# Kernel optimization log

Measured on AMD Instinct MI355X. Metric: run time of the kernel, lower is better.

Reference implementation:

```python
import jax, jax.numpy as jnp
import numpy as np

B = 512      # batch = envs * nagents
M = 32       # nmodels
NAG = 8      # nagents
H = 256      # hidsz
NACT = 16    # nactions


def _lm(x, W, b, ids):
    # LinearMulti: per-example weight selected by model id.
    # x: [B, I], W: [M, I, O], b: [M, O], ids: [B] -> [B, O]
    return jnp.einsum('bi,bio->bo', x, W[ids]) + b[ids]


def setup_inputs() -> dict:
    key = jax.random.key(0)
    ks = jax.random.split(key, 16)
    s = 0.02
    return {
        'comm_in': jax.random.normal(ks[0], (B, NAG, H), jnp.float32),
        'inp': jnp.zeros((B, 1), jnp.int32),  # Embedding table has 1 row -> only index 0 valid
        'prev_hid': jax.random.normal(ks[1], (B, H), jnp.float32),
        'prev_cell': jnp.zeros((B, H), jnp.float32),  # unused in rnn branch, kept for signature fidelity
        'model_ids': jax.random.randint(ks[2], (B,), 0, M),
        # comm2hid LinearMulti (comm_encoder): hidsz -> hidsz
        'Wc': jax.random.normal(ks[3], (M, H, H), jnp.float32) * s,
        'bc': jax.random.normal(ks[4], (M, H), jnp.float32) * s,
        # rnn LinearMulti: hidsz -> hidsz
        'Wr': jax.random.normal(ks[5], (M, H, H), jnp.float32) * s,
        'br': jax.random.normal(ks[6], (M, H), jnp.float32) * s,
        # action LinearMulti: hidsz -> nactions
        'Wa': jax.random.normal(ks[7], (M, H, NACT), jnp.float32) * s,
        'ba': jax.random.normal(ks[8], (M, NACT), jnp.float32) * s,
        # baseline LinearMulti: hidsz -> 1
        'Wb': jax.random.normal(ks[9], (M, H, 1), jnp.float32) * s,
        'bb': jax.random.normal(ks[10], (M, 1), jnp.float32) * s,
        # comm_out LinearMulti (fully_connected): hidsz -> hidsz * nagents
        'Wo': jax.random.normal(ks[11], (M, H, H * NAG), jnp.float32) * s,
        'bo': jax.random.normal(ks[12], (M, H * NAG), jnp.float32) * s,
        # Encoder: Embedding(1, hidsz) + bias
        'lut': jax.random.normal(ks[13], (1, H), jnp.float32) * s,
        'enc_bias': jax.random.normal(ks[14], (H,), jnp.float32) * s,
    }


def reference(comm_in, inp, prev_hid, prev_cell, model_ids,
              Wc, bc, Wr, br, Wa, ba, Wb, bb, Wo, bo, lut, enc_bias):
    # __comm2hid: sum agent messages, then model-id-routed linear
    comm2hid = _lm(jnp.sum(comm_in, axis=1), Wc, bc, model_ids)  # [B, H]
    # Encoder: embedding lookup, sum over token dim, add bias
    enc = jnp.sum(lut[inp], axis=1) + enc_bias                   # [B, H]
    # _rnn: sum of encoder, routed recurrent linear, and comm; tanh gate
    hidstate = jnp.tanh(enc + _lm(prev_hid, Wr, br, model_ids) + comm2hid)
    # __action
    action_prob = jax.nn.softmax(_lm(hidstate, Wa, ba, model_ids), axis=-1)  # [B, NACT]
    baseline = _lm(hidstate, Wb, bb, model_ids)                              # [B, 1]
    # __comm_out (fully_connected): routed linear then divide by nagents-1
    comm_out = _lm(hidstate, Wo, bo, model_ids) / (NAG - 1)                  # [B, H*NAG]
    return (action_prob, baseline, hidstate, comm_out)
```

## Files before the change

kernel.cpp:

```cpp
#include <hip/hip_runtime.h>


constexpr int Bn = 512, Mn = 32, NAGn = 8, Hn = 256, NACTn = 16;
constexpr int On = Hn * NAGn;
constexpr int En = 32;
constexpr int EW = 8;

__device__ __forceinline__ void gl_lds16(const float* g, float* l) {
  __builtin_amdgcn_global_load_lds(
      (const __attribute__((address_space(1))) void*)g,
      (__attribute__((address_space(3))) void*)l, 16, 0, 0);
}


__global__ __launch_bounds__(512) void k_group(const int* __restrict__ ids,
                                               int* __restrict__ list32) {
  __shared__ int scnt[Mn];
  int t = threadIdx.x;
  if (t < Mn) scnt[t] = 0;
  list32[t] = -1;
  list32[t + 512] = -1;
  __syncthreads();
  int m = ids[t];
  int pos = atomicAdd(&scnt[m], 1);
  if (pos < En) list32[m * En + pos] = t;
}

__global__ __launch_bounds__(256) void k_pack(
    const float* __restrict__ comm_in, const float* __restrict__ prev_hid,
    const int* __restrict__ list32, float* __restrict__ xcat) {
  int m = blockIdx.x, half = blockIdx.y;
  int tid = threadIdx.x;
  __shared__ float buf[En][Hn + 1];
  __shared__ int lst[En];
  if (tid < En) lst[tid] = list32[m * En + tid];
  __syncthreads();
  if (half == 0) {
    for (int j = 0; j < En; j++) {
      int e = lst[j];
      float s = 0.f;
      if (e >= 0) {
        const float* cp = comm_in + (size_t)e * NAGn * Hn + tid;
#pragma unroll
        for (int a = 0; a < NAGn; a++) s += cp[a * Hn];
      }
      buf[j][tid] = s;
    }
  } else {
    for (int j = 0; j < En; j++) {
      int e = lst[j];
      buf[j][tid] = (e >= 0) ? prev_hid[e * Hn + tid] : 0.f;
    }
  }
  __syncthreads();
  int j = tid & 31, kr = tid >> 5;
  float* xm = xcat + ((size_t)m * 512 + half * Hn) * En;
  for (int k0 = 0; k0 < Hn; k0 += 8) {
    int k = k0 + kr;
    xm[(size_t)k * En + j] = buf[j][k];
  }
}

__global__ __launch_bounds__(256) void k_lin(
    const float* __restrict__ Wc, const float* __restrict__ Wr,
    const float* __restrict__ xcat, const int* __restrict__ list32,
    float* __restrict__ acc4) {
  int ct = blockIdx.x, kc = blockIdx.y, m = blockIdx.z;
  if (list32[m * En] < 0) return;
  int tid = threadIdx.x, w = tid >> 6, lane = tid & 63;
  __shared__ alignas(16) float xbuf[128 * En];
  __shared__ alignas(16) float wbuf[2][32 * 128];

  const float* W = (kc < 2) ? (Wc + ((size_t)m * Hn + kc * 128) * Hn)
                            : (Wr + ((size_t)m * Hn + (kc - 2) * 128) * Hn);
  const float* wsrc = W + ct * 128;
  const float* xsrc = xcat + ((size_t)m * 512 + kc * 128) * En;
#pragma unroll
  for (int q = 0; q < 4; q++) {
    int c = w * 4 + q;
    gl_lds16(xsrc + c * 256 + lane * 4, xbuf + c * 256);
  }
#pragma unroll
  for (int q = 0; q < 4; q++) {
    int c = w * 4 + q;
    int row = c * 2 + (lane >> 5);
    gl_lds16(wsrc + (size_t)row * Hn + (lane & 31) * 4, wbuf[0] + c * 256);
  }
  bool act = list32[m * En + w * EW] >= 0;
  float2 acc[EW];
#pragma unroll
  for (int j = 0; j < EW; j++) acc[j] = make_float2(0.f, 0.f);
  __syncthreads();

  for (int t = 0; t < 4; t++) {
    if (t < 3) {
      const float* ws2 = wsrc + (size_t)(t + 1) * 32 * Hn;
#pragma unroll
      for (int q = 0; q < 4; q++) {
        int c = w * 4 + q;
        int row = c * 2 + (lane >> 5);
        gl_lds16(ws2 + (size_t)row * Hn + (lane & 31) * 4, wbuf[(t + 1) & 1] + c * 256);
      }
    }
    if (act) {
      const float* wb = wbuf[t & 1] + lane * 2;
      const float* xb = xbuf + (size_t)(t * 32) * En + w * EW;
#pragma unroll 8
      for (int k = 0; k < 32; k++) {
        float2 wv = *(const float2*)(wb + k * 128);
        float4 xa = *(const float4*)(xb + k * En);
        float4 xc = *(const float4*)(xb + k * En + 4);
        acc[0].x += xa.x * wv.x; acc[0].y += xa.x * wv.y;
        acc[1].x += xa.y * wv.x; acc[1].y += xa.y * wv.y;
        acc[2].x += xa.z * wv.x; acc[2].y += xa.z * wv.y;
        acc[3].x += xa.w * wv.x; acc[3].y += xa.w * wv.y;
        acc[4].x += xc.x * wv.x; acc[4].y += xc.x * wv.y;
        acc[5].x += xc.y * wv.x; acc[5].y += xc.y * wv.y;
        acc[6].x += xc.z * wv.x; acc[6].y += xc.z * wv.y;
        acc[7].x += xc.w * wv.x; acc[7].y += xc.w * wv.y;
      }
    }
    __syncthreads();
  }
  if (act) {
    float* ap = acc4 + (((size_t)kc * Mn + m) * En + w * EW) * Hn + ct * 128 + lane * 2;
#pragma unroll
    for (int j = 0; j < EW; j++)
      *(float2*)(ap + (size_t)j * Hn) = acc[j];
  }
}

__global__ __launch_bounds__(256) void k_fin(
    const float* __restrict__ acc4, const float* __restrict__ bc,
    const float* __restrict__ br, const int* __restrict__ inp,
    const float* __restrict__ lut, const float* __restrict__ enc_bias,
    const int* __restrict__ list32, float* __restrict__ hid,
    float* __restrict__ xh) {
  int m = blockIdx.x, cs4 = blockIdx.y;
  int tid = threadIdx.x, lane = tid & 63, jw = tid >> 6;
  int col = cs4 * 64 + lane;
  __shared__ float hb[En][65];
  __shared__ int lst[En];
  if (tid < En) lst[tid] = list32[m * En + tid];
  __syncthreads();
  float bsum = bc[m * Hn + col] + br[m * Hn + col] + enc_bias[col];
  for (int jj = 0; jj < EW; jj++) {
    int j = jw * EW + jj;
    int e = lst[j];
    float h = 0.f;
    if (e >= 0) {
      int tok = inp[e];
      float t = bsum + lut[(size_t)tok * Hn + col];
#pragma unroll
      for (int kc = 0; kc < 4; kc++)
        t += acc4[(((size_t)kc * Mn + m) * En + j) * Hn + col];
      h = tanhf(t);
      hid[(size_t)e * Hn + col] = h;
    }
    hb[j][lane] = h;
  }
  __syncthreads();
  int j2 = tid & 31, kr = tid >> 5;
  for (int k0 = 0; k0 < 64; k0 += 8) {
    int kl = k0 + kr;
    xh[((size_t)m * Hn + cs4 * 64 + kl) * En + j2] = hb[j2][kl];
  }
}

__global__ __launch_bounds__(256) void k_out(
    const float* __restrict__ Wo, const float* __restrict__ xh,
    const float* __restrict__ bo, const int* __restrict__ list32,
    float* __restrict__ comm_out) {
  int ct = blockIdx.x, m = blockIdx.y;
  if (list32[m * En] < 0) return;
  int tid = threadIdx.x, w = tid >> 6, lane = tid & 63;
  __shared__ alignas(16) float xbuf[Hn * En];
  __shared__ alignas(16) float wbuf[2][16 * 128];

  const float* xsrc = xh + (size_t)m * Hn * En;
#pragma unroll
  for (int q = 0; q < 8; q++) {
    int c = w * 8 + q;
    gl_lds16(xsrc + c * 256 + lane * 4, xbuf + c * 256);
  }
  const float* wsrc = Wo + (size_t)m * Hn * On + ct * 128;
#pragma unroll
  for (int q = 0; q < 2; q++) {
    int c = w * 2 + q;
    int row = c * 2 + (lane >> 5);
    gl_lds16(wsrc + (size_t)row * On + (lane & 31) * 4, wbuf[0] + c * 256);
  }
  bool act = list32[m * En + w * EW] >= 0;
  float2 acc[EW];
#pragma unroll
  for (int j = 0; j < EW; j++) acc[j] = make_float2(0.f, 0.f);
  __syncthreads();

  for (int t = 0; t < 16; t++) {
    if (t < 15) {
      const float* ws2 = wsrc + (size_t)(t + 1) * 16 * On;
#pragma unroll
      for (int q = 0; q < 2; q++) {
        int c = w * 2 + q;
        int row = c * 2 + (lane >> 5);
        gl_lds16(ws2 + (size_t)row * On + (lane & 31) * 4, wbuf[(t + 1) & 1] + c * 256);
      }
    }
    if (act) {
      const float* wb = wbuf[t & 1] + lane * 2;
      const float* xb = xbuf + (size_t)(t * 16) * En + w * EW;
#pragma unroll 8
      for (int k = 0; k < 16; k++) {
        float2 wv = *(const float2*)(wb + k * 128);
        float4 xa = *(const float4*)(xb + k * En);
        float4 xc = *(const float4*)(xb + k * En + 4);
        acc[0].x += xa.x * wv.x; acc[0].y += xa.x * wv.y;
        acc[1].x += xa.y * wv.x; acc[1].y += xa.y * wv.y;
        acc[2].x += xa.z * wv.x; acc[2].y += xa.z * wv.y;
        acc[3].x += xa.w * wv.x; acc[3].y += xa.w * wv.y;
        acc[4].x += xc.x * wv.x; acc[4].y += xc.x * wv.y;
        acc[5].x += xc.y * wv.x; acc[5].y += xc.y * wv.y;
        acc[6].x += xc.z * wv.x; acc[6].y += xc.z * wv.y;
        acc[7].x += xc.w * wv.x; acc[7].y += xc.w * wv.y;
      }
    }
    __syncthreads();
  }
  if (act) {
    float2 bv = *(const float2*)(bo + (size_t)m * On + ct * 128 + lane * 2);
    const float inv = 1.f / 7.f;
#pragma unroll
    for (int jj = 0; jj < EW; jj++) {
      int e = list32[m * En + w * EW + jj];
      if (e < 0) continue;
      float2 o;
      o.x = (acc[jj].x + bv.x) * inv;
      o.y = (acc[jj].y + bv.y) * inv;
      *(float2*)(comm_out + (size_t)e * On + ct * 128 + lane * 2) = o;
    }
  }
}

__global__ __launch_bounds__(64) void k_act(
    const float* __restrict__ hid, const float* __restrict__ Wa,
    const float* __restrict__ ba, const float* __restrict__ Wb,
    const float* __restrict__ bb, const int* __restrict__ ids,
    float* __restrict__ aprob, float* __restrict__ bl) {
  int b = blockIdx.x;
  int m = ids[b];
  int l = threadIdx.x;
  int o = l & 15;
  int kk = l >> 4;

  const float* wap = Wa + (size_t)m * Hn * NACTn + l;
  const float* hbase = hid + (size_t)b * Hn;
  float al = 0.f;
  for (int w16 = 0; w16 < 4; w16++) {
    float wv[16], hv[16];
#pragma unroll
    for (int il = 0; il < 16; il++) wv[il] = wap[(w16 * 16 + il) * 64];
#pragma unroll
    for (int il = 0; il < 16; il++) hv[il] = hbase[w16 * 64 + il * 4 + kk];
#pragma unroll
    for (int il = 0; il < 16; il++) al += wv[il] * hv[il];
  }
  al += __shfl_xor(al, 16);
  al += __shfl_xor(al, 32);
  al += ba[m * NACTn + o];

  float mx = al;
  mx = fmaxf(mx, __shfl_xor(mx, 1));
  mx = fmaxf(mx, __shfl_xor(mx, 2));
  mx = fmaxf(mx, __shfl_xor(mx, 4));
  mx = fmaxf(mx, __shfl_xor(mx, 8));
  float ex = expf(al - mx);
  float sm = ex;
  sm += __shfl_xor(sm, 1);
  sm += __shfl_xor(sm, 2);
  sm += __shfl_xor(sm, 4);
  sm += __shfl_xor(sm, 8);
  if (l < 16) aprob[b * NACTn + l] = ex / sm;

  float pb = 0.f;
  const float* wbp = Wb + (size_t)m * Hn;
  {
    float wv[4], hv[4];
#pragma unroll
    for (int k = 0; k < 4; k++) { wv[k] = wbp[l + k * 64]; hv[k] = hbase[l + k * 64]; }
#pragma unroll
    for (int k = 0; k < 4; k++) pb += wv[k] * hv[k];
  }
  pb += __shfl_xor(pb, 1);
  pb += __shfl_xor(pb, 2);
  pb += __shfl_xor(pb, 4);
  pb += __shfl_xor(pb, 8);
  pb += __shfl_xor(pb, 16);
  pb += __shfl_xor(pb, 32);
  if (l == 0) bl[b] = pb + bb[m];
}

extern "C" void kernel_launch(void* const* d_in, const int* in_sizes, int n_in,
                              void* d_out, int out_size, void* d_ws, size_t ws_size,
                              hipStream_t stream) {
  const float* comm_in  = (const float*)d_in[0];
  const int*   inp      = (const int*)d_in[1];
  const float* prev_hid = (const float*)d_in[2];
  const int*   ids      = (const int*)d_in[4];
  const float* Wc = (const float*)d_in[5];
  const float* bc = (const float*)d_in[6];
  const float* Wr = (const float*)d_in[7];
  const float* br = (const float*)d_in[8];
  const float* Wa = (const float*)d_in[9];
  const float* ba = (const float*)d_in[10];
  const float* Wb = (const float*)d_in[11];
  const float* bb = (const float*)d_in[12];
  const float* Wo = (const float*)d_in[13];
  const float* bo = (const float*)d_in[14];
  const float* lut      = (const float*)d_in[15];
  const float* enc_bias = (const float*)d_in[16];

  float* out      = (float*)d_out;
  float* aprob    = out;
  float* bl       = out + Bn * NACTn;
  float* hid      = out + Bn * NACTn + Bn;
  float* comm_out = hid + Bn * Hn;

  char* ws = (char*)d_ws;
  int*   list32 = (int*)ws;
  float* xcat   = (float*)(ws + 4096);
  float* xh     = (float*)(ws + 4096 + 2097152);
  float* acc4   = (float*)(ws + 4096 + 3145728);

  k_group<<<1, 512, 0, stream>>>(ids, list32);
  k_pack<<<dim3(Mn, 2), 256, 0, stream>>>(comm_in, prev_hid, list32, xcat);
  k_lin<<<dim3(2, 4, Mn), 256, 0, stream>>>(Wc, Wr, xcat, list32, acc4);
  k_fin<<<dim3(Mn, 4), 256, 0, stream>>>(acc4, bc, br, inp, lut, enc_bias,
                                         list32, hid, xh);
  k_out<<<dim3(16, Mn), 256, 0, stream>>>(Wo, xh, bo, list32, comm_out);
  k_act<<<Bn, 64, 0, stream>>>(hid, Wa, ba, Wb, bb, ids, aprob, bl);
}
```

Before: 191.0 us.

## Fuse grouping and packing into GEMM kernels, merge hidden/action kernels

```diff
diff --git a/kernel.cpp b/kernel.cpp
--- a/kernel.cpp
+++ b/kernel.cpp
@@ -5,6 +5,7 @@
 constexpr int On = Hn * NAGn;
 constexpr int En = 32;
 constexpr int EW = 8;
+constexpr int XS = 40;
 
 __device__ __forceinline__ void gl_lds16(const float* g, float* l) {
   __builtin_amdgcn_global_load_lds(
@@ -12,176 +13,187 @@
       (__attribute__((address_space(3))) void*)l, 16, 0, 0);
 }
 
-
-__global__ __launch_bounds__(512) void k_group(const int* __restrict__ ids,
-                                               int* __restrict__ list32) {
-  __shared__ int scnt[Mn];
-  int t = threadIdx.x;
-  if (t < Mn) scnt[t] = 0;
-  list32[t] = -1;
-  list32[t + 512] = -1;
-  __syncthreads();
-  int m = ids[t];
-  int pos = atomicAdd(&scnt[m], 1);
-  if (pos < En) list32[m * En + pos] = t;
-}
-
-__global__ __launch_bounds__(256) void k_pack(
-    const float* __restrict__ comm_in, const float* __restrict__ prev_hid,
-    const int* __restrict__ list32, float* __restrict__ xcat) {
-  int m = blockIdx.x, half = blockIdx.y;
-  int tid = threadIdx.x;
-  __shared__ float buf[En][Hn + 1];
-  __shared__ int lst[En];
-  if (tid < En) lst[tid] = list32[m * En + tid];
-  __syncthreads();
-  if (half == 0) {
-    for (int j = 0; j < En; j++) {
-      int e = lst[j];
-      float s = 0.f;
-      if (e >= 0) {
-        const float* cp = comm_in + (size_t)e * NAGn * Hn + tid;
-#pragma unroll
-        for (int a = 0; a < NAGn; a++) s += cp[a * Hn];
-      }
-      buf[j][tid] = s;
-    }
-  } else {
-    for (int j = 0; j < En; j++) {
-      int e = lst[j];
-      buf[j][tid] = (e >= 0) ? prev_hid[e * Hn + tid] : 0.f;
-    }
-  }
-  __syncthreads();
-  int j = tid & 31, kr = tid >> 5;
-  float* xm = xcat + ((size_t)m * 512 + half * Hn) * En;
-  for (int k0 = 0; k0 < Hn; k0 += 8) {
-    int k = k0 + kr;
-    xm[(size_t)k * En + j] = buf[j][k];
-  }
-}
+__device__ __forceinline__ void build_group(const int* __restrict__ ids, int m,
+                                            int* lst, int* cnt, int tid) {
+  if (tid < En) lst[tid] = -1;
+  if (tid == 0) *cnt = 0;
+  __syncthreads();
+  for (int i = tid; i < Bn; i += 256) {
+    if (ids[i] == m) {
+      int p = atomicAdd(cnt, 1);
+      if (p < En) lst[p] = i;
+    }
+  }
+  __syncthreads();
+}
+
 
 __global__ __launch_bounds__(256) void k_lin(
     const float* __restrict__ Wc, const float* __restrict__ Wr,
-    const float* __restrict__ xcat, const int* __restrict__ list32,
-    float* __restrict__ acc4) {
+    const float* __restrict__ comm_in, const float* __restrict__ prev_hid,
+    const int* __restrict__ ids, float* __restrict__ acc8) {
   int ct = blockIdx.x, kc = blockIdx.y, m = blockIdx.z;
-  if (list32[m * En] < 0) return;
   int tid = threadIdx.x, w = tid >> 6, lane = tid & 63;
-  __shared__ alignas(16) float xbuf[128 * En];
+  __shared__ int lst[En];
+  __shared__ int cnt;
+  __shared__ alignas(16) float xs[64 * XS];
   __shared__ alignas(16) float wbuf[2][32 * 128];
 
-  const float* W = (kc < 2) ? (Wc + ((size_t)m * Hn + kc * 128) * Hn)
-                            : (Wr + ((size_t)m * Hn + (kc - 2) * 128) * Hn);
-  const float* wsrc = W + ct * 128;
-  const float* xsrc = xcat + ((size_t)m * 512 + kc * 128) * En;
-#pragma unroll
-  for (int q = 0; q < 4; q++) {
-    int c = w * 4 + q;
-    gl_lds16(xsrc + c * 256 + lane * 4, xbuf + c * 256);
+  build_group(ids, m, lst, &cnt, tid);
+  if (cnt == 0) return;
+
+  int kb = (kc & 3) * 64;
+  const float* W = ((kc < 4) ? Wc : Wr) + (size_t)m * Hn * Hn + (size_t)kb * Hn + ct * 128;
+
+  int k = lane, j0 = w * EW;
+#pragma unroll
+  for (int jj = 0; jj < EW; jj++) {
+    int j = j0 + jj, e = lst[j];
+    float v = 0.f;
+    if (e >= 0) {
+      if (kc < 4) {
+        const float* cp = comm_in + (size_t)e * NAGn * Hn + kb + k;
+#pragma unroll
+        for (int a = 0; a < NAGn; a++) v += cp[a * Hn];
+      } else {
+        v = prev_hid[(size_t)e * Hn + kb + k];
+      }
+    }
+    xs[k * XS + j] = v;
   }
 #pragma unroll
   for (int q = 0; q < 4; q++) {
     int c = w * 4 + q;
     int row = c * 2 + (lane >> 5);
-    gl_lds16(wsrc + (size_t)row * Hn + (lane & 31) * 4, wbuf[0] + c * 256);
-  }
-  bool act = list32[m * En + w * EW] >= 0;
+    gl_lds16(W + (size_t)row * Hn + (lane & 31) * 4, wbuf[0] + c * 256);
+  }
   float2 acc[EW];
 #pragma unroll
   for (int j = 0; j < EW; j++) acc[j] = make_float2(0.f, 0.f);
   __syncthreads();
 
-  for (int t = 0; t < 4; t++) {
-    if (t < 3) {
-      const float* ws2 = wsrc + (size_t)(t + 1) * 32 * Hn;
+  for (int t = 0; t < 2; t++) {
+    if (t == 0) {
 #pragma unroll
       for (int q = 0; q < 4; q++) {
         int c = w * 4 + q;
-        int row = c * 2 + (lane >> 5);
-        gl_lds16(ws2 + (size_t)row * Hn + (lane & 31) * 4, wbuf[(t + 1) & 1] + c * 256);
+        int row = 32 + c * 2 + (lane >> 5);
+        gl_lds16(W + (size_t)row * Hn + (lane & 31) * 4, wbuf[1] + c * 256);
       }
     }
-    if (act) {
-      const float* wb = wbuf[t & 1] + lane * 2;
-      const float* xb = xbuf + (size_t)(t * 32) * En + w * EW;
+    const float* wb = wbuf[t] + lane * 2;
+    const float* xb = xs + (size_t)(t * 32) * XS + j0;
 #pragma unroll 8
-      for (int k = 0; k < 32; k++) {
-        float2 wv = *(const float2*)(wb + k * 128);
-        float4 xa = *(const float4*)(xb + k * En);
-        float4 xc = *(const float4*)(xb + k * En + 4);
-        acc[0].x += xa.x * wv.x; acc[0].y += xa.x * wv.y;
-        acc[1].x += xa.y * wv.x; acc[1].y += xa.y * wv.y;
-        acc[2].x += xa.z * wv.x; acc[2].y += xa.z * wv.y;
-        acc[3].x += xa.w * wv.x; acc[3].y += xa.w * wv.y;
-        acc[4].x += xc.x * wv.x; acc[4].y += xc.x * wv.y;
-        acc[5].x += xc.y * wv.x; acc[5].y += xc.y * wv.y;
-        acc[6].x += xc.z * wv.x; acc[6].y += xc.z * wv.y;
-        acc[7].x += xc.w * wv.x; acc[7].y += xc.w * wv.y;
-      }
+    for (int kk = 0; kk < 32; kk++) {
+      float2 wv = *(const float2*)(wb + kk * 128);
+      float4 xa = *(const float4*)(xb + kk * XS);
+      float4 xc = *(const float4*)(xb + kk * XS + 4);
+      acc[0].x += xa.x * wv.x; acc[0].y += xa.x * wv.y;
+      acc[1].x += xa.y * wv.x; acc[1].y += xa.y * wv.y;
+      acc[2].x += xa.z * wv.x; acc[2].y += xa.z * wv.y;
+      acc[3].x += xa.w * wv.x; acc[3].y += xa.w * wv.y;
+      acc[4].x += xc.x * wv.x; acc[4].y += xc.x * wv.y;
+      acc[5].x += xc.y * wv.x; acc[5].y += xc.y * wv.y;
+      acc[6].x += xc.z * wv.x; acc[6].y += xc.z * wv.y;
+      acc[7].x += xc.w * wv.x; acc[7].y += xc.w * wv.y;
     }
     __syncthreads();
   }
-  if (act) {
-    float* ap = acc4 + (((size_t)kc * Mn + m) * En + w * EW) * Hn + ct * 128 + lane * 2;
-#pragma unroll
-    for (int j = 0; j < EW; j++)
-      *(float2*)(ap + (size_t)j * Hn) = acc[j];
-  }
-}
-
-__global__ __launch_bounds__(256) void k_fin(
-    const float* __restrict__ acc4, const float* __restrict__ bc,
+#pragma unroll
+  for (int jj = 0; jj < EW; jj++) {
+    int e = lst[j0 + jj];
+    if (e < 0) continue;
+    *(float2*)(acc8 + ((size_t)kc * Bn + e) * Hn + ct * 128 + lane * 2) = acc[jj];
+  }
+}
+
+__global__ __launch_bounds__(256) void k_hidact(
+    const float* __restrict__ acc8, const float* __restrict__ bc,
     const float* __restrict__ br, const int* __restrict__ inp,
     const float* __restrict__ lut, const float* __restrict__ enc_bias,
-    const int* __restrict__ list32, float* __restrict__ hid,
-    float* __restrict__ xh) {
-  int m = blockIdx.x, cs4 = blockIdx.y;
-  int tid = threadIdx.x, lane = tid & 63, jw = tid >> 6;
-  int col = cs4 * 64 + lane;
-  __shared__ float hb[En][65];
-  __shared__ int lst[En];
-  if (tid < En) lst[tid] = list32[m * En + tid];
-  __syncthreads();
-  float bsum = bc[m * Hn + col] + br[m * Hn + col] + enc_bias[col];
-  for (int jj = 0; jj < EW; jj++) {
-    int j = jw * EW + jj;
-    int e = lst[j];
-    float h = 0.f;
-    if (e >= 0) {
-      int tok = inp[e];
-      float t = bsum + lut[(size_t)tok * Hn + col];
-#pragma unroll
-      for (int kc = 0; kc < 4; kc++)
-        t += acc4[(((size_t)kc * Mn + m) * En + j) * Hn + col];
-      h = tanhf(t);
-      hid[(size_t)e * Hn + col] = h;
-    }
-    hb[j][lane] = h;
-  }
-  __syncthreads();
-  int j2 = tid & 31, kr = tid >> 5;
-  for (int k0 = 0; k0 < 64; k0 += 8) {
-    int kl = k0 + kr;
-    xh[((size_t)m * Hn + cs4 * 64 + kl) * En + j2] = hb[j2][kl];
+    const int* __restrict__ ids, const float* __restrict__ Wa,
+    const float* __restrict__ ba, const float* __restrict__ Wb,
+    const float* __restrict__ bb, float* __restrict__ hid,
+    float* __restrict__ aprob, float* __restrict__ bl) {
+  int e = blockIdx.x, tid = threadIdx.x;
+  int m = ids[e];
+  __shared__ float hs[Hn];
+  float t = bc[m * Hn + tid] + br[m * Hn + tid] + enc_bias[tid] +
+            lut[(size_t)inp[e] * Hn + tid];
+#pragma unroll
+  for (int kc = 0; kc < 8; kc++)
+    t += acc8[((size_t)kc * Bn + e) * Hn + tid];
+  float h = tanhf(t);
+  hid[(size_t)e * Hn + tid] = h;
+  hs[tid] = h;
+  __syncthreads();
+  if (tid < 64) {
+    int l = tid, o = l & 15, kk = l >> 4;
+    const float* wap = Wa + (size_t)m * Hn * NACTn + l;
+    float al = 0.f;
+    for (int w16 = 0; w16 < 4; w16++) {
+      float wv[16], hv[16];
+#pragma unroll
+      for (int il = 0; il < 16; il++) wv[il] = wap[(w16 * 16 + il) * 64];
+#pragma unroll
+      for (int il = 0; il < 16; il++) hv[il] = hs[w16 * 64 + il * 4 + kk];
+#pragma unroll
+      for (int il = 0; il < 16; il++) al += wv[il] * hv[il];
+    }
+    al += __shfl_xor(al, 16);
+    al += __shfl_xor(al, 32);
+    al += ba[m * NACTn + o];
+
+    float mx = al;
+    mx = fmaxf(mx, __shfl_xor(mx, 1));
+    mx = fmaxf(mx, __shfl_xor(mx, 2));
+    mx = fmaxf(mx, __shfl_xor(mx, 4));
+    mx = fmaxf(mx, __shfl_xor(mx, 8));
+    float ex = expf(al - mx);
+    float sm = ex;
+    sm += __shfl_xor(sm, 1);
+    sm += __shfl_xor(sm, 2);
+    sm += __shfl_xor(sm, 4);
+    sm += __shfl_xor(sm, 8);
+    if (l < 16) aprob[e * NACTn + l] = ex / sm;
+
+    float pb = 0.f;
+    const float* wbp = Wb + (size_t)m * Hn;
+    {
+      float wv[4], hv[4];
+#pragma unroll
+      for (int k = 0; k < 4; k++) { wv[k] = wbp[l + k * 64]; hv[k] = hs[l + k * 64]; }
+#pragma unroll
+      for (int k = 0; k < 4; k++) pb += wv[k] * hv[k];
+    }
+    pb += __shfl_xor(pb, 1);
+    pb += __shfl_xor(pb, 2);
+    pb += __shfl_xor(pb, 4);
+    pb += __shfl_xor(pb, 8);
+    pb += __shfl_xor(pb, 16);
+    pb += __shfl_xor(pb, 32);
+    if (l == 0) bl[e] = pb + bb[m];
   }
 }
 
 __global__ __launch_bounds__(256) void k_out(
-    const float* __restrict__ Wo, const float* __restrict__ xh,
-    const float* __restrict__ bo, const int* __restrict__ list32,
+    const float* __restrict__ Wo, const float* __restrict__ hid,
+    const float* __restrict__ bo, const int* __restrict__ ids,
     float* __restrict__ comm_out) {
   int ct = blockIdx.x, m = blockIdx.y;
-  if (list32[m * En] < 0) return;
   int tid = threadIdx.x, w = tid >> 6, lane = tid & 63;
-  __shared__ alignas(16) float xbuf[Hn * En];
+  __shared__ int lst[En];
+  __shared__ int cnt;
+  __shared__ alignas(16) float xs[Hn * XS];
   __shared__ alignas(16) float wbuf[2][16 * 128];
 
-  const float* xsrc = xh + (size_t)m * Hn * En;
-#pragma unroll
-  for (int q = 0; q < 8; q++) {
-    int c = w * 8 + q;
-    gl_lds16(xsrc + c * 256 + lane * 4, xbuf + c * 256);
+  build_group(ids, m, lst, &cnt, tid);
+  if (cnt == 0) return;
+
+  for (int j = 0; j < En; j++) {
+    int e = lst[j];
+    float v = (e >= 0) ? hid[(size_t)e * Hn + tid] : 0.f;
+    xs[tid * XS + j] = v;
   }
   const float* wsrc = Wo + (size_t)m * Hn * On + ct * 128;
 #pragma unroll
@@ -190,7 +202,7 @@
     int row = c * 2 + (lane >> 5);
     gl_lds16(wsrc + (size_t)row * On + (lane & 31) * 4, wbuf[0] + c * 256);
   }
-  bool act = list32[m * En + w * EW] >= 0;
+  int j0 = w * EW;
   float2 acc[EW];
 #pragma unroll
   for (int j = 0; j < EW; j++) acc[j] = make_float2(0.f, 0.f);
@@ -206,97 +218,35 @@
         gl_lds16(ws2 + (size_t)row * On + (lane & 31) * 4, wbuf[(t + 1) & 1] + c * 256);
       }
     }
-    if (act) {
-      const float* wb = wbuf[t & 1] + lane * 2;
-      const float* xb = xbuf + (size_t)(t * 16) * En + w * EW;
+    const float* wb = wbuf[t & 1] + lane * 2;
+    const float* xb = xs + (size_t)(t * 16) * XS + j0;
 #pragma unroll 8
-      for (int k = 0; k < 16; k++) {
-        float2 wv = *(const float2*)(wb + k * 128);
-        float4 xa = *(const float4*)(xb + k * En);
-        float4 xc = *(const float4*)(xb + k * En + 4);
-        acc[0].x += xa.x * wv.x; acc[0].y += xa.x * wv.y;
-        acc[1].x += xa.y * wv.x; acc[1].y += xa.y * wv.y;
-        acc[2].x += xa.z * wv.x; acc[2].y += xa.z * wv.y;
-        acc[3].x += xa.w * wv.x; acc[3].y += xa.w * wv.y;
-        acc[4].x += xc.x * wv.x; acc[4].y += xc.x * wv.y;
-        acc[5].x += xc.y * wv.x; acc[5].y += xc.y * wv.y;
-        acc[6].x += xc.z * wv.x; acc[6].y += xc.z * wv.y;
-        acc[7].x += xc.w * wv.x; acc[7].y += xc.w * wv.y;
-      }
+    for (int k = 0; k < 16; k++) {
+      float2 wv = *(const float2*)(wb + k * 128);
+      float4 xa = *(const float4*)(xb + k * XS);
+      float4 xc = *(const float4*)(xb + k * XS + 4);
+      acc[0].x += xa.x * wv.x; acc[0].y += xa.x * wv.y;
+      acc[1].x += xa.y * wv.x; acc[1].y += xa.y * wv.y;
+      acc[2].x += xa.z * wv.x; acc[2].y += xa.z * wv.y;
+      acc[3].x += xa.w * wv.x; acc[3].y += xa.w * wv.y;
+      acc[4].x += xc.x * wv.x; acc[4].y += xc.x * wv.y;
+      acc[5].x += xc.y * wv.x; acc[5].y += xc.y * wv.y;
+      acc[6].x += xc.z * wv.x; acc[6].y += xc.z * wv.y;
+      acc[7].x += xc.w * wv.x; acc[7].y += xc.w * wv.y;
     }
     __syncthreads();
   }
-  if (act) {
-    float2 bv = *(const float2*)(bo + (size_t)m * On + ct * 128 + lane * 2);
-    const float inv = 1.f / 7.f;
-#pragma unroll
-    for (int jj = 0; jj < EW; jj++) {
-      int e = list32[m * En + w * EW + jj];
-      if (e < 0) continue;
-      float2 o;
-      o.x = (acc[jj].x + bv.x) * inv;
-      o.y = (acc[jj].y + bv.y) * inv;
-      *(float2*)(comm_out + (size_t)e * On + ct * 128 + lane * 2) = o;
-    }
-  }
-}
-
-__global__ __launch_bounds__(64) void k_act(
-    const float* __restrict__ hid, const float* __restrict__ Wa,
-    const float* __restrict__ ba, const float* __restrict__ Wb,
-    const float* __restrict__ bb, const int* __restrict__ ids,
-    float* __restrict__ aprob, float* __restrict__ bl) {
-  int b = blockIdx.x;
-  int m = ids[b];
-  int l = threadIdx.x;
-  int o = l & 15;
-  int kk = l >> 4;
-
-  const float* wap = Wa + (size_t)m * Hn * NACTn + l;
-  const float* hbase = hid + (size_t)b * Hn;
-  float al = 0.f;
-  for (int w16 = 0; w16 < 4; w16++) {
-    float wv[16], hv[16];
-#pragma unroll
-    for (int il = 0; il < 16; il++) wv[il] = wap[(w16 * 16 + il) * 64];
-#pragma unroll
-    for (int il = 0; il < 16; il++) hv[il] = hbase[w16 * 64 + il * 4 + kk];
-#pragma unroll
-    for (int il = 0; il < 16; il++) al += wv[il] * hv[il];
-  }
-  al += __shfl_xor(al, 16);
-  al += __shfl_xor(al, 32);
-  al += ba[m * NACTn + o];
-
-  float mx = al;
-  mx = fmaxf(mx, __shfl_xor(mx, 1));
-  mx = fmaxf(mx, __shfl_xor(mx, 2));
-  mx = fmaxf(mx, __shfl_xor(mx, 4));
-  mx = fmaxf(mx, __shfl_xor(mx, 8));
-  float ex = expf(al - mx);
-  float sm = ex;
-  sm += __shfl_xor(sm, 1);
-  sm += __shfl_xor(sm, 2);
-  sm += __shfl_xor(sm, 4);
-  sm += __shfl_xor(sm, 8);
-  if (l < 16) aprob[b * NACTn + l] = ex / sm;
-
-  float pb = 0.f;
-  const float* wbp = Wb + (size_t)m * Hn;
-  {
-    float wv[4], hv[4];
-#pragma unroll
-    for (int k = 0; k < 4; k++) { wv[k] = wbp[l + k * 64]; hv[k] = hbase[l + k * 64]; }
-#pragma unroll
-    for (int k = 0; k < 4; k++) pb += wv[k] * hv[k];
-  }
-  pb += __shfl_xor(pb, 1);
-  pb += __shfl_xor(pb, 2);
-  pb += __shfl_xor(pb, 4);
-  pb += __shfl_xor(pb, 8);
-  pb += __shfl_xor(pb, 16);
-  pb += __shfl_xor(pb, 32);
-  if (l == 0) bl[b] = pb + bb[m];
+  float2 bv = *(const float2*)(bo + (size_t)m * On + ct * 128 + lane * 2);
+  const float inv = 1.f / 7.f;
+#pragma unroll
+  for (int jj = 0; jj < EW; jj++) {
+    int e = lst[j0 + jj];
+    if (e < 0) continue;
+    float2 o;
+    o.x = (acc[jj].x + bv.x) * inv;
+    o.y = (acc[jj].y + bv.y) * inv;
+    *(float2*)(comm_out + (size_t)e * On + ct * 128 + lane * 2) = o;
+  }
 }
 
 extern "C" void kernel_launch(void* const* d_in, const int* in_sizes, int n_in,
@@ -325,17 +275,10 @@
   float* hid      = out + Bn * NACTn + Bn;
   float* comm_out = hid + Bn * Hn;
 
-  char* ws = (char*)d_ws;
-  int*   list32 = (int*)ws;
-  float* xcat   = (float*)(ws + 4096);
-  float* xh     = (float*)(ws + 4096 + 2097152);
-  float* acc4   = (float*)(ws + 4096 + 3145728);
-
-  k_group<<<1, 512, 0, stream>>>(ids, list32);
-  k_pack<<<dim3(Mn, 2), 256, 0, stream>>>(comm_in, prev_hid, list32, xcat);
-  k_lin<<<dim3(2, 4, Mn), 256, 0, stream>>>(Wc, Wr, xcat, list32, acc4);
-  k_fin<<<dim3(Mn, 4), 256, 0, stream>>>(acc4, bc, br, inp, lut, enc_bias,
-                                         list32, hid, xh);
-  k_out<<<dim3(16, Mn), 256, 0, stream>>>(Wo, xh, bo, list32, comm_out);
-  k_act<<<Bn, 64, 0, stream>>>(hid, Wa, ba, Wb, bb, ids, aprob, bl);
-}
+  float* acc8 = (float*)d_ws;
+
+  k_lin<<<dim3(2, 8, Mn), 256, 0, stream>>>(Wc, Wr, comm_in, prev_hid, ids, acc8);
+  k_hidact<<<Bn, 256, 0, stream>>>(acc8, bc, br, inp, lut, enc_bias, ids,
+                                   Wa, ba, Wb, bb, hid, aprob, bl);
+  k_out<<<dim3(16, Mn), 256, 0, stream>>>(Wo, hid, bo, ids, comm_out);
+}
```

After: 173.1 us. 1.1x faster.
